# Performance work log

Measured on AMD Instinct MI355X. Metric: run time of the kernel, lower is better.

The kernel has to match this reference:

```python
import jax, jax.numpy as jnp
import numpy as np

B, S, E, H, V, T, L = 64, 512, 512, 512, 32000, 2, 1


def setup_inputs() -> dict:
    key = jax.random.key(0)
    ks = jax.random.split(key, 12)
    # xavier_normal std for h0/c0 of shape (L, B, H): fan_in=B*H, fan_out=L*H
    xav = float(np.sqrt(2.0 / (B * H + L * H)))
    s = 1.0 / float(np.sqrt(H))  # pytorch LSTM default uniform bound
    return {
        "sentence": jax.random.randint(ks[0], (B, S), 0, V, dtype=jnp.int64),
        "h0": jax.random.normal(ks[1], (L, B, H), jnp.float32) * xav,
        "c0": jax.random.normal(ks[2], (L, B, H), jnp.float32) * xav,
        "emb": jax.random.normal(ks[3], (V, E), jnp.float32),
        "W_ih": jax.random.uniform(ks[4], (4 * H, E), jnp.float32, -s, s),
        "W_hh": jax.random.uniform(ks[5], (4 * H, H), jnp.float32, -s, s),
        "b_ih": jax.random.uniform(ks[6], (4 * H,), jnp.float32, -s, s),
        "b_hh": jax.random.uniform(ks[7], (4 * H,), jnp.float32, -s, s),
        "W_lin": jax.random.uniform(ks[8], (T, H), jnp.float32, -s, s),
        "b_lin": jax.random.uniform(ks[9], (T,), jnp.float32, -s, s),
    }


def reference(sentence, h0, c0, emb, W_ih, W_hh, b_ih, b_hh, W_lin, b_lin):
    x = emb[sentence]                                   # [B,S,E]
    # precompute input-to-gate projections for all timesteps
    xg = jnp.einsum("bse,ge->bsg", x, W_ih) + (b_ih + b_hh)  # [B,S,4H]

    def step(carry, xt):
        h, c = carry                                    # [B,H] each
        g = xt + h @ W_hh.T                             # [B,4H]
        i, f, gc, o = jnp.split(g, 4, axis=-1)          # torch gate order i,f,g,o
        i = jax.nn.sigmoid(i)
        f = jax.nn.sigmoid(f)
        gc = jnp.tanh(gc)
        o = jax.nn.sigmoid(o)
        c = f * c + i * gc
        h = o * jnp.tanh(c)
        return (h, c), h

    (hn, cn), hs = jax.lax.scan(step, (h0[0], c0[0]), xg.transpose(1, 0, 2))
    lstm_out = hs.transpose(1, 0, 2)                    # [B,S,H]
    # dropout is identity at inference; torch code indexes drop[-1,:,:] =
    # LAST BATCH SAMPLE (batch_first=True quirk) -> [S,H]
    last = lstm_out[-1]                                 # [S,H]
    return last @ W_lin.T + b_lin                       # [S,T]
```

## Files before the change

kernel.cpp:

```cpp
#include <hip/hip_runtime.h>


typedef float f32x4 __attribute__((ext_vector_type(4)));
typedef unsigned long long u64;

#define NB 64

#define HIDX(e) ((((e) >> 4) * 20) + ((e) & 15))

__global__ __launch_bounds__(256) void xg_gemm_k(
    const int* __restrict__ sent, const float* __restrict__ emb,
    const float* __restrict__ W_ih, const float* __restrict__ b_ih,
    const float* __restrict__ b_hh, float* __restrict__ xg)
{
    __shared__ float As[16][65];
    __shared__ float Bs[16][65];
    __shared__ int aidx[64];
    const int tid = threadIdx.x;
    const int t0 = blockIdx.x * 64;
    const int n0 = blockIdx.y * 64;
    if (tid < 64) aidx[tid] = sent[63 * 512 + t0 + tid];
    __syncthreads();

    const int kk = tid & 15;
    const int mm = tid >> 4;
    const int tx = tid & 15, ty = tid >> 4;
    float acc[4][4] = {};

    for (int kb = 0; kb < 512; kb += 16) {
        #pragma unroll
        for (int j = 0; j < 4; j++) {
            int m = mm + j * 16;
            As[kk][m] = emb[(size_t)aidx[m] * 512 + kb + kk];
            Bs[kk][m] = W_ih[(size_t)(n0 + m) * 512 + kb + kk];
        }
        __syncthreads();
        #pragma unroll
        for (int k = 0; k < 16; k++) {
            float a[4], bv[4];
            #pragma unroll
            for (int i = 0; i < 4; i++) a[i] = As[k][ty * 4 + i];
            #pragma unroll
            for (int j = 0; j < 4; j++) bv[j] = Bs[k][tx * 4 + j];
            #pragma unroll
            for (int i = 0; i < 4; i++)
                #pragma unroll
                for (int j = 0; j < 4; j++)
                    acc[i][j] += a[i] * bv[j];
        }
        __syncthreads();
    }

    #pragma unroll
    for (int i = 0; i < 4; i++) {
        int t = t0 + ty * 4 + i;
        #pragma unroll
        for (int j = 0; j < 4; j++) {
            int col = n0 + tx * 4 + j;
            xg[(size_t)t * 2048 + col] = acc[i][j] + b_ih[col] + b_hh[col];
        }
    }
}

__global__ __launch_bounds__(256, 1) void lstm_seq_k(
    const float* __restrict__ h0, const float* __restrict__ c0,
    const float* __restrict__ W_hh, const float* __restrict__ xg,
    float* __restrict__ hs,
    u64* __restrict__ sA, u64* __restrict__ sB)
{
    __shared__ float hb[2][648];

    const int tid = threadIdx.x;
    const int b = blockIdx.x;
    const int cg = tid & 31;
    const int rg = tid >> 5;

    int grow[4];
    #pragma unroll
    for (int r = 0; r < 4; ++r)
        grow[r] = r * 512 + b * 8 + rg;

    f32x4 w[4][4];
    #pragma unroll
    for (int r = 0; r < 4; ++r)
        #pragma unroll
        for (int cq = 0; cq < 4; ++cq)
            w[r][cq] = *(const f32x4*)&W_hh[(size_t)grow[r] * 512 + cg * 16 + cq * 4];

    float creg = c0[63 * 512 + b * 8 + rg];

    for (int t = 0; t < 512; ++t) {
        #pragma unroll
        for (int r = 0; r < 4; ++r)
            asm volatile("" : "+v"(w[r][0]), "+v"(w[r][1]),
                              "+v"(w[r][2]), "+v"(w[r][3]));

        const int p = t & 1;

        float xgp[4];
        if (cg == 0) {
            #pragma unroll
            for (int r = 0; r < 4; ++r)
                xgp[r] = xg[(size_t)t * 2048 + grow[r]];
        }

        if (t == 0) {
            hb[p][HIDX(tid)]       = h0[63 * 512 + tid];
            hb[p][HIDX(tid + 256)] = h0[63 * 512 + tid + 256];
        } else {
            u64* src = ((t - 1) & 1) ? sB : sA;
            u64* p0 = &src[tid];
            u64* p1 = &src[tid + 256];
            const unsigned expt = (unsigned)t;
            u64 v0, v1;
            for (;;) {
                v0 = __hip_atomic_load(p0, __ATOMIC_RELAXED, __HIP_MEMORY_SCOPE_AGENT);
                v1 = __hip_atomic_load(p1, __ATOMIC_RELAXED, __HIP_MEMORY_SCOPE_AGENT);
                if ((unsigned)(v0 >> 32) == expt &&
                    (unsigned)(v1 >> 32) == expt) break;
            }
            hb[p][HIDX(tid)]       = __uint_as_float((unsigned)v0);
            hb[p][HIDX(tid + 256)] = __uint_as_float((unsigned)v1);
        }
        __syncthreads();

        f32x4 hv[4];
        #pragma unroll
        for (int cq = 0; cq < 4; ++cq)
            hv[cq] = *(const f32x4*)&hb[p][cg * 20 + cq * 4];

        float acc[4];
        #pragma unroll
        for (int r = 0; r < 4; ++r) {
            float s = 0.f;
            #pragma unroll
            for (int cq = 0; cq < 4; ++cq) {
                s += w[r][cq].x * hv[cq].x;
                s += w[r][cq].y * hv[cq].y;
                s += w[r][cq].z * hv[cq].z;
                s += w[r][cq].w * hv[cq].w;
            }
            acc[r] = s;
        }

        #pragma unroll
        for (int r = 0; r < 4; ++r) {
            #pragma unroll
            for (int m = 16; m >= 1; m >>= 1)
                acc[r] += __shfl_xor(acc[r], m, 64);
        }

        if (cg == 0) {
            float gi = acc[0] + xgp[0];
            float gf = acc[1] + xgp[1];
            float gc = acc[2] + xgp[2];
            float go = acc[3] + xgp[3];
            float ii = 1.f / (1.f + __expf(-gi));
            float ff = 1.f / (1.f + __expf(-gf));
            float cc = 1.f - 2.f / (__expf(2.f * gc) + 1.f);
            float oo = 1.f / (1.f + __expf(-go));
            float cn = ff * creg + ii * cc;
            creg = cn;
            float th = 1.f - 2.f / (__expf(2.f * cn) + 1.f);
            float hval = oo * th;

            hs[(size_t)t * 512 + b * 8 + rg] = hval;

            u64* dst = (t & 1) ? sB : sA;
            u64 pv = ((u64)(unsigned)(t + 1) << 32) |
                     (u64)__float_as_uint(hval);
            __hip_atomic_store(&dst[b * 8 + rg], pv,
                               __ATOMIC_RELAXED, __HIP_MEMORY_SCOPE_AGENT);
        }
    }
}

__global__ __launch_bounds__(256) void final_linear_k(
    const float* __restrict__ hs, const float* __restrict__ W_lin,
    const float* __restrict__ b_lin, float* __restrict__ out)
{
    const int tid = threadIdx.x;
    const int wave = tid >> 6;
    const int lane = tid & 63;
    const int s = blockIdx.x * 4 + wave;
    const float* h = hs + (size_t)s * 512;
    float a0 = 0.f, a1 = 0.f;
    #pragma unroll
    for (int k0 = 0; k0 < 512; k0 += 64) {
        float hv = h[k0 + lane];
        a0 += hv * W_lin[k0 + lane];
        a1 += hv * W_lin[512 + k0 + lane];
    }
    #pragma unroll
    for (int m = 32; m >= 1; m >>= 1) {
        a0 += __shfl_xor(a0, m, 64);
        a1 += __shfl_xor(a1, m, 64);
    }
    if (lane == 0) {
        out[s * 2]     = a0 + b_lin[0];
        out[s * 2 + 1] = a1 + b_lin[1];
    }
}

extern "C" void kernel_launch(void* const* d_in, const int* in_sizes, int n_in,
                              void* d_out, int out_size, void* d_ws, size_t ws_size,
                              hipStream_t stream)
{
    const int*   sent  = (const int*)d_in[0];
    const float* h0    = (const float*)d_in[1];
    const float* c0    = (const float*)d_in[2];
    const float* emb   = (const float*)d_in[3];
    const float* W_ih  = (const float*)d_in[4];
    const float* W_hh  = (const float*)d_in[5];
    const float* b_ih  = (const float*)d_in[6];
    const float* b_hh  = (const float*)d_in[7];
    const float* W_lin = (const float*)d_in[8];
    const float* b_lin = (const float*)d_in[9];
    float* out = (float*)d_out;

    char* ws = (char*)d_ws;
    float* xg = (float*)ws;
    float* hs = (float*)(ws + 4 * 1024 * 1024);
    u64* sA = (u64*)(ws + 5 * 1024 * 1024);
    u64* sB = (u64*)(ws + 5 * 1024 * 1024 + 4096);

    hipMemsetAsync(sA, 0, 2 * 4096, stream);

    dim3 g1(8, 32);
    xg_gemm_k<<<g1, 256, 0, stream>>>(sent, emb, W_ih, b_ih, b_hh, xg);
    lstm_seq_k<<<NB, 256, 0, stream>>>(h0, c0, W_hh, xg, hs, sA, sB);
    final_linear_k<<<128, 256, 0, stream>>>(hs, W_lin, b_lin, out);
}
```

Measured before the change: 1.124 ms.

## Halve LSTM recurrence blocks to 32 with 16 hidden units per block

```diff
diff --git a/kernel.cpp b/kernel.cpp
--- a/kernel.cpp
+++ b/kernel.cpp
@@ -4,9 +4,7 @@
 typedef float f32x4 __attribute__((ext_vector_type(4)));
 typedef unsigned long long u64;
 
-#define NB 64
-
-#define HIDX(e) ((((e) >> 4) * 20) + ((e) & 15))
+#define NB 32
 
 __global__ __launch_bounds__(256) void xg_gemm_k(
     const int* __restrict__ sent, const float* __restrict__ emb,
@@ -68,33 +66,34 @@
     float* __restrict__ hs,
     u64* __restrict__ sA, u64* __restrict__ sB)
 {
-    __shared__ float hb[2][648];
+    __shared__ float hb[2][16 * 36];
 
     const int tid = threadIdx.x;
     const int b = blockIdx.x;
-    const int cg = tid & 31;
-    const int rg = tid >> 5;
+    const int cg = tid & 15;
+    const int j  = tid >> 4;
 
     int grow[4];
     #pragma unroll
     for (int r = 0; r < 4; ++r)
-        grow[r] = r * 512 + b * 8 + rg;
-
-    f32x4 w[4][4];
+        grow[r] = r * 512 + b * 16 + j;
+
+    f32x4 w[4][8];
     #pragma unroll
     for (int r = 0; r < 4; ++r)
         #pragma unroll
-        for (int cq = 0; cq < 4; ++cq)
-            w[r][cq] = *(const f32x4*)&W_hh[(size_t)grow[r] * 512 + cg * 16 + cq * 4];
-
-    float creg = c0[63 * 512 + b * 8 + rg];
+        for (int cq = 0; cq < 8; ++cq)
+            w[r][cq] = *(const f32x4*)&W_hh[(size_t)grow[r] * 512 + cg * 32 + cq * 4];
+
+    #pragma unroll
+    for (int r = 0; r < 4; ++r)
+        asm volatile("" : "+v"(w[r][0]), "+v"(w[r][1]), "+v"(w[r][2]),
+                          "+v"(w[r][3]), "+v"(w[r][4]), "+v"(w[r][5]),
+                          "+v"(w[r][6]), "+v"(w[r][7]));
+
+    float creg = c0[63 * 512 + b * 16 + j];
 
     for (int t = 0; t < 512; ++t) {
-        #pragma unroll
-        for (int r = 0; r < 4; ++r)
-            asm volatile("" : "+v"(w[r][0]), "+v"(w[r][1]),
-                              "+v"(w[r][2]), "+v"(w[r][3]));
-
         const int p = t & 1;
 
         float xgp[4];
@@ -105,36 +104,40 @@
         }
 
         if (t == 0) {
-            hb[p][HIDX(tid)]       = h0[63 * 512 + tid];
-            hb[p][HIDX(tid + 256)] = h0[63 * 512 + tid + 256];
+            const int e0 = 2 * tid;
+            hb[p][(e0 >> 5) * 36 + (e0 & 31)]     = h0[63 * 512 + e0];
+            hb[p][(e0 >> 5) * 36 + (e0 & 31) + 1] = h0[63 * 512 + e0 + 1];
         } else {
             u64* src = ((t - 1) & 1) ? sB : sA;
-            u64* p0 = &src[tid];
-            u64* p1 = &src[tid + 256];
+            u64* p0 = &src[2 * tid];
+            u64* p1 = &src[2 * tid + 1];
             const unsigned expt = (unsigned)t;
-            u64 v0, v1;
+            u64 v0 = __hip_atomic_load(p0, __ATOMIC_RELAXED, __HIP_MEMORY_SCOPE_AGENT);
+            u64 v1 = __hip_atomic_load(p1, __ATOMIC_RELAXED, __HIP_MEMORY_SCOPE_AGENT);
             for (;;) {
-                v0 = __hip_atomic_load(p0, __ATOMIC_RELAXED, __HIP_MEMORY_SCOPE_AGENT);
-                v1 = __hip_atomic_load(p1, __ATOMIC_RELAXED, __HIP_MEMORY_SCOPE_AGENT);
+                u64 n0 = __hip_atomic_load(p0, __ATOMIC_RELAXED, __HIP_MEMORY_SCOPE_AGENT);
+                u64 n1 = __hip_atomic_load(p1, __ATOMIC_RELAXED, __HIP_MEMORY_SCOPE_AGENT);
                 if ((unsigned)(v0 >> 32) == expt &&
                     (unsigned)(v1 >> 32) == expt) break;
+                v0 = n0; v1 = n1;
             }
-            hb[p][HIDX(tid)]       = __uint_as_float((unsigned)v0);
-            hb[p][HIDX(tid + 256)] = __uint_as_float((unsigned)v1);
+            const int e0 = 2 * tid;
+            hb[p][(e0 >> 5) * 36 + (e0 & 31)]     = __uint_as_float((unsigned)v0);
+            hb[p][(e0 >> 5) * 36 + (e0 & 31) + 1] = __uint_as_float((unsigned)v1);
         }
         __syncthreads();
 
-        f32x4 hv[4];
-        #pragma unroll
-        for (int cq = 0; cq < 4; ++cq)
-            hv[cq] = *(const f32x4*)&hb[p][cg * 20 + cq * 4];
+        f32x4 hv[8];
+        #pragma unroll
+        for (int cq = 0; cq < 8; ++cq)
+            hv[cq] = *(const f32x4*)&hb[p][cg * 36 + cq * 4];
 
         float acc[4];
         #pragma unroll
         for (int r = 0; r < 4; ++r) {
             float s = 0.f;
             #pragma unroll
-            for (int cq = 0; cq < 4; ++cq) {
+            for (int cq = 0; cq < 8; ++cq) {
                 s += w[r][cq].x * hv[cq].x;
                 s += w[r][cq].y * hv[cq].y;
                 s += w[r][cq].z * hv[cq].z;
@@ -146,7 +149,7 @@
         #pragma unroll
         for (int r = 0; r < 4; ++r) {
             #pragma unroll
-            for (int m = 16; m >= 1; m >>= 1)
+            for (int m = 8; m >= 1; m >>= 1)
                 acc[r] += __shfl_xor(acc[r], m, 64);
         }
 
@@ -164,12 +167,12 @@
             float th = 1.f - 2.f / (__expf(2.f * cn) + 1.f);
             float hval = oo * th;
 
-            hs[(size_t)t * 512 + b * 8 + rg] = hval;
+            hs[(size_t)t * 512 + b * 16 + j] = hval;
 
             u64* dst = (t & 1) ? sB : sA;
             u64 pv = ((u64)(unsigned)(t + 1) << 32) |
                      (u64)__float_as_uint(hval);
-            __hip_atomic_store(&dst[b * 8 + rg], pv,
+            __hip_atomic_store(&dst[b * 16 + j], pv,
                                __ATOMIC_RELAXED, __HIP_MEMORY_SCOPE_AGENT);
         }
     }
```

Result: slower. 1.312 ms (+16.7%).
